# Performance work log

Hardware: AMD Instinct MI355X
Metric: run time of the kernel (lower is better)

The kernel has to match this reference:

```python
import jax, jax.numpy as jnp
import numpy as np

PI = 3.141592653589793


def _conv2d(x, w, b=None, pad=0, groups=1):
    out = jax.lax.conv_general_dilated(
        x, w, (1, 1), ((pad, pad), (pad, pad)),
        dimension_numbers=('NCHW', 'OIHW', 'NCHW'), feature_group_count=groups)
    if b is not None:
        out = out + b[None, :, None, None]
    return out


def _l2norm(x, eps=1e-12):
    # torch F.normalize(p=2, dim=1)
    n = jnp.sqrt(jnp.sum(x * x, axis=1, keepdims=True))
    return x / jnp.maximum(n, eps)


def dense_sift(x):
    # Kornia DenseSIFTDescriptor defaults: 8 angular bins, 4x4 spatial bins,
    # spatial_bin_size=4, stride=1, padding=1, rootsift=True, clipval=0.2.
    eps = 1e-10
    nbins = 8
    # SpatialGradient('diff', normalized=False) with replicate padding:
    px = jnp.pad(x, ((0, 0), (0, 0), (0, 0), (1, 1)), mode='edge')
    gx = px[..., 2:] - px[..., :-2]
    py = jnp.pad(x, ((0, 0), (0, 0), (1, 1), (0, 0)), mode='edge')
    gy = py[:, :, 2:, :] - py[:, :, :-2, :]
    mag = jnp.sqrt(gx * gx + gy * gy + eps)
    ori = jnp.arctan2(gy, gx + eps) + 2.0 * PI
    o_big = nbins * ori / (2.0 * PI)
    bo0f = jnp.floor(o_big)
    wo1 = o_big - bo0f
    bo0 = jnp.mod(bo0f, nbins)
    bo1 = jnp.mod(bo0 + 1.0, nbins)
    w0 = (1.0 - wo1) * mag
    w1 = wo1 * mag
    bins = jnp.arange(nbins, dtype=x.dtype).reshape(1, nbins, 1, 1)
    # soft-assign gradient magnitude into 8 orientation bins  (B,8,H,W)
    ang = (bo0 == bins) * w0 + (bo1 == bins) * w1
    # AvgPool2d(4, stride=1, pad=2, count_include_pad=True) -> (B,8,H+1,W+1)
    avg_k = jnp.ones((nbins, 1, 4, 4), x.dtype) / 16.0
    pooled = _conv2d(ang, avg_k, pad=2, groups=nbins)
    # PoolingConv: identity-reshape 4x4 kernel, pad=1 -> 16 shifted copies of 8 chans
    B, _, Hp, Wp = pooled.shape
    H, W = Hp - 1, Wp - 1
    pp = jnp.pad(pooled, ((0, 0), (0, 0), (1, 1), (1, 1)))
    shifts = jnp.stack(
        [pp[:, :, i:i + H, j:j + W] for i in range(4) for j in range(4)], axis=2)
    out = shifts.reshape(B, nbins * 16, H, W)  # channel n = d*16 + i*4 + j
    out = jnp.clip(_l2norm(out), 0.0, 0.2)
    out = _l2norm(out)
    # rootsift: sqrt(L1-normalize + eps)
    l1 = jnp.sum(jnp.abs(out), axis=1, keepdims=True)
    return jnp.sqrt(out / jnp.maximum(l1, 1e-12) + eps)


def joint_bilateral_blur(x, guidance, ksize=5, sigma_color=0.1, sigma_space=1.5):
    # Kornia joint_bilateral_blur, border='reflect', color_distance='l1'
    r = ksize // 2
    ax = jnp.arange(ksize, dtype=x.dtype) - r
    g1 = jnp.exp(-(ax * ax) / (2.0 * sigma_space ** 2))
    g1 = g1 / jnp.sum(g1)
    space_k = jnp.outer(g1, g1)
    H, W = x.shape[-2], x.shape[-1]
    px = jnp.pad(x, ((0, 0), (0, 0), (r, r), (r, r)), mode='reflect')
    pg = jnp.pad(guidance, ((0, 0), (0, 0), (r, r), (r, r)), mode='reflect')
    num = jnp.zeros_like(x)
    den = jnp.zeros((x.shape[0], 1, H, W), x.dtype)
    inv = -0.5 / (sigma_color ** 2)
    for dy in range(ksize):
        for dx in range(ksize):
            gw = pg[:, :, dy:dy + H, dx:dx + W]
            cd = jnp.square(jnp.sum(jnp.abs(gw - guidance), axis=1, keepdims=True))
            k = space_k[dy, dx] * jnp.exp(inv * cd)
            num = num + px[:, :, dy:dy + H, dx:dx + W] * k
            den = den + k
    return num / den


def setup_inputs() -> dict:
    key = jax.random.key(0)
    ks = jax.random.split(key, 7)
    B, H, W = 4, 270, 512
    x = jax.random.uniform(ks[0], (B, 1, H, W), dtype=jnp.float32)
    def winit(k, shape):
        fan_in = shape[1] * shape[2] * shape[3]
        return jax.random.normal(k, shape, dtype=jnp.float32) / np.sqrt(fan_in)
    return {
        'x': x,
        'conv1_w': winit(ks[1], (32, 128, 5, 5)),
        'conv1_b': jax.random.normal(ks[2], (32,), dtype=jnp.float32) * 0.01,
        'conv2_w': winit(ks[3], (8, 32, 3, 3)),
        'conv2_b': jax.random.normal(ks[4], (8,), dtype=jnp.float32) * 0.01,
        'conv3_w': winit(ks[5], (2, 8, 5, 5)),
        'conv3_b': jax.random.normal(ks[6], (2,), dtype=jnp.float32) * 0.01,
    }


def reference(x, conv1_w, conv1_b, conv2_w, conv2_b, conv3_w, conv3_b):
    orig = x
    f = dense_sift(x)
    f = jax.nn.relu(_conv2d(f, conv1_w, conv1_b, pad=2))
    f = jax.nn.relu(_conv2d(f, conv2_w, conv2_b, pad=1))
    f = _conv2d(f, conv3_w, conv3_b, pad=2)
    f = joint_bilateral_blur(f, jnp.concatenate([orig, orig], axis=1))
    u = f[:, 0]
    u = jnp.clip((u - u.min()) / (u.max() - u.min() + 1e-6), 0.0, 1.0)
    u = u * (0.436 * 2.0) - 0.436
    v = f[:, 1]
    v = jnp.clip((v - v.min()) / (v.max() - v.min() + 1e-6), 0.0, 1.0)
    v = v * (0.615 * 2.0) - 0.615
    y = orig[:, 0]
    r = y + 1.14 * v
    g = y - 0.396 * u - 0.581 * v
    b = y + 2.029 * u
    return jnp.stack([r, g, b], axis=1)
```

## Files before the change

kernel.cpp:

```cpp
#include <hip/hip_runtime.h>
#include <hip/hip_bf16.h>

typedef __hip_bfloat16 bf16;
typedef __attribute__((ext_vector_type(8))) short short8v;
typedef __attribute__((ext_vector_type(16))) float f32x16;

#define HH 270
#define WW 512
#define BB 4
#define HP 271
#define WP 513
#define NPIX (HH*WW)
#define NPOOL (HP*WP)
#define TWO_PI 6.28318530717958647692f
#define PLANE ((size_t)BB*NPIX*16)

__global__ void k_wprep(const float* __restrict__ w1, const float* __restrict__ w2,
                        const float* __restrict__ w3, short* __restrict__ apack,
                        float* __restrict__ wT2, float* __restrict__ wT3,
                        float* __restrict__ zp) {
    int stride = gridDim.x * blockDim.x;
    int t0 = blockIdx.x * blockDim.x + threadIdx.x;
    for (int i = t0; i < 1024; i += stride) zp[i] = 0.f;
    for (int i = t0; i < 8*25*64*8; i += stride) {
        int idx = i;
        int j    = idx & 7;  idx >>= 3;
        int lane = idx & 63; idx >>= 6;
        int t    = idx % 25;
        int ck   = idx / 25;
        int o = lane & 31;
        int c = ck*16 + (lane >> 5)*8 + j;
        float v = w1[o*3200 + c*25 + t];
        bf16 h = __float2bfloat16(v);
        apack[i] = *reinterpret_cast<short*>(&h);
    }
    for (int i = t0; i < 288*8;  i += stride) { int ck = i >> 3, o = i & 7;  wT2[i] = w2[o*288  + ck]; }
    for (int i = t0; i < 200*2;  i += stride) { int ck = i >> 1, o = i & 1;  wT3[i] = w3[o*200  + ck]; }
}

__global__ __launch_bounds__(256) void k_pool(const float* __restrict__ x,
                                              float* __restrict__ pooled) {
    __shared__ float hist[8][19][20];
    const int tx = threadIdx.x & 15, ty = threadIdx.x >> 4;
    const int j0 = blockIdx.x * 16, i0 = blockIdx.y * 16, b = blockIdx.z;
    const float* xb = x + (size_t)b * NPIX;

    for (int i = threadIdx.x; i < 8*19*20; i += 256) ((float*)hist)[i] = 0.f;
    __syncthreads();

    for (int i = threadIdx.x; i < 361; i += 256) {
        int lh = i / 19, lw = i - lh*19;
        int hh = i0 + lh - 2, ww = j0 + lw - 2;
        if (hh >= 0 && hh < HH && ww >= 0 && ww < WW) {
            float gx = xb[hh*WW + (ww+1 < WW ? ww+1 : WW-1)] - xb[hh*WW + (ww-1 >= 0 ? ww-1 : 0)];
            float gy = xb[(hh+1 < HH ? hh+1 : HH-1)*WW + ww] - xb[(hh-1 >= 0 ? hh-1 : 0)*WW + ww];
            float mag  = sqrtf(gx*gx + gy*gy + 1e-10f);
            float ori  = atan2f(gy, gx + 1e-10f) + TWO_PI;
            float obig = ori * (8.0f / TWO_PI);
            float b0f  = floorf(obig);
            float wo1  = obig - b0f;
            int ib0 = ((int)b0f) & 7;
            int ib1 = (ib0 + 1) & 7;
            hist[ib0][lh][lw] += (1.0f - wo1) * mag;
            hist[ib1][lh][lw] += wo1 * mag;
        }
    }
    __syncthreads();

    int i = i0 + ty, j = j0 + tx;
    if (i < HP && j < WP) {
        float a[8];
        #pragma unroll
        for (int c = 0; c < 8; ++c) a[c] = 0.f;
        #pragma unroll
        for (int di = 0; di < 4; ++di)
            #pragma unroll
            for (int dj = 0; dj < 4; ++dj) {
                #pragma unroll
                for (int c = 0; c < 8; ++c)
                    a[c] += hist[c][ty+di][tx+dj];
            }
        float* pb = pooled + (size_t)b*8*NPOOL + i*WP + j;
        const float s = 1.0f/16.0f;
        #pragma unroll
        for (int c = 0; c < 8; ++c) pb[c*NPOOL] = a[c]*s;
    }
}

__global__ __launch_bounds__(256) void k_feat(const float* __restrict__ pooled,
                                              short* __restrict__ f2) {
    __shared__ float T[8][19][19];
    const int tx = threadIdx.x & 15, ty = threadIdx.x >> 4;
    const int w0 = blockIdx.x * 16, h0 = blockIdx.y * 16, b = blockIdx.z;
    const float* pb = pooled + (size_t)b*8*NPOOL;

    for (int i = threadIdx.x; i < 8*361; i += 256) {
        int c = i / 361; int r = i - c*361; int lh = r / 19, lw = r - lh*19;
        int ph = h0 + lh - 1, pw = w0 + lw - 1;
        float v = 0.f;
        if (ph >= 0 && ph < HP && pw >= 0 && pw < WP)
            v = pb[c*NPOOL + ph*WP + pw];
        T[c][lh][lw] = v;
    }
    __syncthreads();

    float s2 = 0.f;
    #pragma unroll
    for (int c = 0; c < 8; ++c)
        #pragma unroll
        for (int i = 0; i < 4; ++i)
            #pragma unroll
            for (int j = 0; j < 4; ++j) {
                float u = T[c][ty+i][tx+j];
                s2 += u*u;
            }
    float inv1 = 1.0f / fmaxf(sqrtf(s2), 1e-12f);

    float sv2 = 0.f, sv1 = 0.f;
    #pragma unroll
    for (int c = 0; c < 8; ++c)
        #pragma unroll
        for (int i = 0; i < 4; ++i)
            #pragma unroll
            for (int j = 0; j < 4; ++j) {
                float u = T[c][ty+i][tx+j];
                float v = fminf(u*inv1, 0.2f);
                sv2 += v*v; sv1 += v;
            }
    float inv2  = 1.0f / fmaxf(sqrtf(sv2), 1e-12f);
    float invl1 = 1.0f / fmaxf(sv1 * inv2, 1e-12f);

    int outv[64];
    #pragma unroll
    for (int c = 0; c < 8; ++c)
        #pragma unroll
        for (int i = 0; i < 4; ++i)
            #pragma unroll
            for (int jj = 0; jj < 2; ++jj) {
                float u0 = T[c][ty+i][tx+jj*2];
                float u1 = T[c][ty+i][tx+jj*2+1];
                float v0 = fminf(u0*inv1, 0.2f) * inv2;
                float v1 = fminf(u1*inv1, 0.2f) * inv2;
                float fo0 = sqrtf(v0*invl1 + 1e-10f);
                float fo1 = sqrtf(v1*invl1 + 1e-10f);
                bf16 hb0 = __float2bfloat16(fo0);
                bf16 hb1 = __float2bfloat16(fo1);
                unsigned lo = *reinterpret_cast<unsigned short*>(&hb0);
                unsigned hi = *reinterpret_cast<unsigned short*>(&hb1);
                outv[c*8 + i*2 + jj] = (int)(lo | (hi << 16));
            }

    int h = h0 + ty, w = w0 + tx;
    if (h < HH) {
        const size_t pix = (size_t)b*NPIX + h*WW + w;
        #pragma unroll
        for (int ck = 0; ck < 8; ++ck) {
            int4* fb = reinterpret_cast<int4*>(f2 + (size_t)ck*PLANE + pix*16);
            int4 v0, v1;
            v0.x = outv[ck*8+0]; v0.y = outv[ck*8+1]; v0.z = outv[ck*8+2]; v0.w = outv[ck*8+3];
            v1.x = outv[ck*8+4]; v1.y = outv[ck*8+5]; v1.z = outv[ck*8+6]; v1.w = outv[ck*8+7];
            fb[0] = v0; fb[1] = v1;
        }
    }
}

__global__ __launch_bounds__(256) void k_conv1(const short* __restrict__ f2,
        const short* __restrict__ apack, const float* __restrict__ bias,
        short* __restrict__ c1o, const float* __restrict__ zp) {
    __shared__ short S[2][17408];
    const int tid = threadIdx.x;
    const int l   = tid & 63;
    const int wid = tid >> 6;
    const int n      = blockIdx.x;
    const int xcd    = n & 7;
    const int t_     = n >> 3;
    const int within = t_ & 7;
    const int g      = (t_ >> 3)*8 + xcd;
    const int b      = g / 34;
    const int ypair  = g - b*34;
    const int h0     = (ypair*2 + (within >> 2)) * 4;
    const int w0     = (within & 3) * 128;
    const int c32 = l & 31;
    const int ksel = l >> 5;

    f32x16 acc0 = {0.f};
    f32x16 acc1 = {0.f};
    f32x16 acc2 = {0.f};
    f32x16 acc3 = {0.f};

    auto STAGE = [&](int ck, int buf) {
        const short* plane = f2 + (size_t)ck*PLANE;
        for (int s = tid; s < 2176; s += 256) {
            int pr   = s / 272;
            int r    = s - pr*272;
            int px   = r >> 1;
            int half = r & 1;
            int gh = h0 + pr - 2, gw = w0 + px - 2;
            const void* src = (gh >= 0 && gh < HH && gw >= 0 && gw < WW)
                ? (const void*)(plane + (((size_t)b*HH + gh)*WW + gw)*16 + half*8)
                : (const void*)zp;
            short* dst = &S[buf][0] + (size_t)(s & ~63) * 8;
            __builtin_amdgcn_global_load_lds(
                (const __attribute__((address_space(1))) void*)src,
                (__attribute__((address_space(3))) void*)dst, 16, 0, 0);
        }
    };

    STAGE(0, 0);
    __syncthreads();

    for (int ck = 0; ck < 8; ++ck) {
        const int buf = ck & 1;
        if (ck < 7) STAGE(ck + 1, buf ^ 1);

        const short* Sb = &S[buf][0];
        #pragma unroll
        for (int kx = 0; kx < 5; ++kx) {
            const int px = wid*32 + c32 + kx;
            const short* bp = Sb + (size_t)px*16 + (size_t)ksel*8;
            short8v Bf[8];
            #pragma unroll
            for (int pr = 0; pr < 8; ++pr)
                Bf[pr] = *reinterpret_cast<const short8v*>(bp + pr*2176);
            #pragma unroll
            for (int ky = 0; ky < 5; ++ky) {
                const short* ap = apack + ((size_t)(ck*25 + ky*5 + kx)*64 + l)*8;
                short8v A = *reinterpret_cast<const short8v*>(ap);
                acc0 = __builtin_amdgcn_mfma_f32_32x32x16_bf16(A, Bf[ky+0], acc0, 0, 0, 0);
                acc1 = __builtin_amdgcn_mfma_f32_32x32x16_bf16(A, Bf[ky+1], acc1, 0, 0, 0);
                acc2 = __builtin_amdgcn_mfma_f32_32x32x16_bf16(A, Bf[ky+2], acc2, 0, 0, 0);
                acc3 = __builtin_amdgcn_mfma_f32_32x32x16_bf16(A, Bf[ky+3], acc3, 0, 0, 0);
            }
        }
        __syncthreads();
    }

    const int px = w0 + wid*32 + c32;
    #pragma unroll
    for (int r = 0; r < 4; ++r) {
        int h = h0 + r;
        if (h < HH) {
            const f32x16& A = (r==0) ? acc0 : (r==1) ? acc1 : (r==2) ? acc2 : acc3;
            const size_t rowbase = ((size_t)b*HH + h)*4;
            #pragma unroll
            for (int q = 0; q < 4; ++q) {
                short4 pk;
                short* pkp = (short*)&pk;
                #pragma unroll
                for (int j = 0; j < 4; ++j) {
                    float v = fmaxf(A[q*4 + j] + bias[q*8 + 4*ksel + j], 0.f);
                    bf16 hb = __float2bfloat16(v);
                    pkp[j] = *reinterpret_cast<short*>(&hb);
                }
                *reinterpret_cast<short4*>(c1o + ((rowbase + q)*WW + px)*8 + ksel*4) = pk;
            }
        }
    }
}

__global__ __launch_bounds__(256) void k_conv2(const short* __restrict__ in,
        const float* __restrict__ wT, const float* __restrict__ bias,
        float* __restrict__ out) {
    __shared__ float tile[8][18][18];
    int tx = threadIdx.x & 15, ty = threadIdx.x >> 4;
    int h0 = blockIdx.y * 16, w0 = blockIdx.x * 16, b = blockIdx.z;
    float acc[8];
    #pragma unroll
    for (int o = 0; o < 8; ++o) acc[o] = 0.f;

    for (int cc = 0; cc < 4; ++cc) {
        __syncthreads();
        for (int t = threadIdx.x; t < 324; t += 256) {
            int lh = t / 18, lw = t - lh*18;
            int gh = h0 + lh - 1, gw = w0 + lw - 1;
            if (gh >= 0 && gh < HH && gw >= 0 && gw < WW) {
                short8v v = *reinterpret_cast<const short8v*>(
                    in + (((size_t)b*HH + gh)*4 + cc)*WW*8 + (size_t)gw*8);
                #pragma unroll
                for (int c = 0; c < 8; ++c) {
                    unsigned u = ((unsigned)(unsigned short)v[c]) << 16;
                    tile[c][lh][lw] = *reinterpret_cast<float*>(&u);
                }
            } else {
                #pragma unroll
                for (int c = 0; c < 8; ++c) tile[c][lh][lw] = 0.f;
            }
        }
        __syncthreads();
        for (int c = 0; c < 8; ++c) {
            #pragma unroll
            for (int ky = 0; ky < 3; ++ky) {
                #pragma unroll
                for (int kx = 0; kx < 3; ++kx) {
                    float v = tile[c][ty+ky][tx+kx];
                    const float* wp = wT + (((cc*8+c)*9) + ky*3 + kx)*8;
                    #pragma unroll
                    for (int o = 0; o < 8; ++o) acc[o] = fmaf(v, wp[o], acc[o]);
                }
            }
        }
    }
    int h = h0 + ty, w = w0 + tx;
    if (h < HH) {
        float* op = out + (size_t)b*8*NPIX + h*WW + w;
        #pragma unroll
        for (int o = 0; o < 8; ++o) op[(size_t)o*NPIX] = fmaxf(acc[o] + bias[o], 0.f);
    }
}

__global__ __launch_bounds__(256) void k_conv3(const float* __restrict__ in,
        const float* __restrict__ wT, const float* __restrict__ bias,
        float* __restrict__ out) {
    __shared__ float tile[8][20][20];
    int tx = threadIdx.x & 15, ty = threadIdx.x >> 4;
    int h0 = blockIdx.y * 16, w0 = blockIdx.x * 16, b = blockIdx.z;
    float acc0 = 0.f, acc1 = 0.f;

    for (int t = threadIdx.x; t < 8*400; t += 256) {
        int c = t / 400; int r = t - c*400; int lh = r / 20, lw = r - lh*20;
        int gh = h0 + lh - 2, gw = w0 + lw - 2;
        float v = 0.f;
        if (gh >= 0 && gh < HH && gw >= 0 && gw < WW)
            v = in[((size_t)(b*8 + c))*NPIX + gh*WW + gw];
        tile[c][lh][lw] = v;
    }
    __syncthreads();
    for (int c = 0; c < 8; ++c) {
        for (int ky = 0; ky < 5; ++ky) {
            #pragma unroll
            for (int kx = 0; kx < 5; ++kx) {
                float v = tile[c][ty+ky][tx+kx];
                const float* wp = wT + ((c*25) + ky*5 + kx)*2;
                acc0 = fmaf(v, wp[0], acc0);
                acc1 = fmaf(v, wp[1], acc1);
            }
        }
    }
    int h = h0 + ty, w = w0 + tx;
    if (h < HH) {
        float* op = out + (size_t)b*2*NPIX + h*WW + w;
        op[0]    = acc0 + bias[0];
        op[NPIX] = acc1 + bias[1];
    }
}

__device__ __forceinline__ int refl(int i, int n) {
    if (i < 0) i = -i;
    if (i >= n) i = 2*n - 2 - i;
    return i;
}

__global__ void k_bilat(const float* __restrict__ c3, const float* __restrict__ x,
                        float* __restrict__ outb) {
    int idx = blockIdx.x * blockDim.x + threadIdx.x;
    if (idx >= BB*NPIX) return;
    int b = idx / NPIX;
    int p = idx - b*NPIX;
    int h = p / WW, w = p - h*WW;
    const float* xb = x + (size_t)b*NPIX;
    const float* f0 = c3 + (size_t)b*2*NPIX;
    const float* f1 = f0 + NPIX;

    float e1 = expf(-1.0f/4.5f), e2 = expf(-4.0f/4.5f);
    float sden = 1.0f + 2.f*e1 + 2.f*e2;
    float g1v[5] = { e2/sden, e1/sden, 1.0f/sden, e1/sden, e2/sden };

    float g = xb[p];
    float num0 = 0.f, num1 = 0.f, den = 0.f;
    #pragma unroll
    for (int dy = 0; dy < 5; ++dy) {
        int hh = refl(h + dy - 2, HH);
        #pragma unroll
        for (int dx = 0; dx < 5; ++dx) {
            int wc = refl(w + dx - 2, WW);
            float gs = xb[hh*WW + wc];
            float d = gs - g;
            float k = g1v[dy] * g1v[dx] * expf(-200.0f * d * d);
            num0 += f0[hh*WW + wc] * k;
            num1 += f1[hh*WW + wc] * k;
            den  += k;
        }
    }
    float invd = 1.0f / den;
    outb[(size_t)b*2*NPIX + p]        = num0 * invd;
    outb[(size_t)b*2*NPIX + NPIX + p] = num1 * invd;
}

__global__ void k_minmax1(const float* __restrict__ blur, float4* __restrict__ partial) {
    float umin = 3.0e38f, umax = -3.0e38f, vmin = 3.0e38f, vmax = -3.0e38f;
    for (int i = blockIdx.x*blockDim.x + threadIdx.x; i < BB*NPIX; i += gridDim.x*blockDim.x) {
        int b = i / NPIX; int p = i - b*NPIX;
        float u = blur[(size_t)b*2*NPIX + p];
        float v = blur[(size_t)b*2*NPIX + NPIX + p];
        umin = fminf(umin, u); umax = fmaxf(umax, u);
        vmin = fminf(vmin, v); vmax = fmaxf(vmax, v);
    }
    #pragma unroll
    for (int off = 32; off > 0; off >>= 1) {
        umin = fminf(umin, __shfl_down(umin, off));
        umax = fmaxf(umax, __shfl_down(umax, off));
        vmin = fminf(vmin, __shfl_down(vmin, off));
        vmax = fmaxf(vmax, __shfl_down(vmax, off));
    }
    __shared__ float4 sm[4];
    int lane = threadIdx.x & 63, wid = threadIdx.x >> 6;
    if (lane == 0) sm[wid] = make_float4(umin, umax, vmin, vmax);
    __syncthreads();
    if (threadIdx.x == 0) {
        float4 r = sm[0];
        for (int k = 1; k < 4; ++k) {
            r.x = fminf(r.x, sm[k].x); r.y = fmaxf(r.y, sm[k].y);
            r.z = fminf(r.z, sm[k].z); r.w = fmaxf(r.w, sm[k].w);
        }
        partial[blockIdx.x] = r;
    }
}

__global__ void k_minmax2(const float4* __restrict__ partial, float* __restrict__ sc) {
    float4 p = partial[threadIdx.x];
    #pragma unroll
    for (int off = 32; off > 0; off >>= 1) {
        p.x = fminf(p.x, __shfl_down(p.x, off));
        p.y = fmaxf(p.y, __shfl_down(p.y, off));
        p.z = fminf(p.z, __shfl_down(p.z, off));
        p.w = fmaxf(p.w, __shfl_down(p.w, off));
    }
    __shared__ float4 sm[2];
    if ((threadIdx.x & 63) == 0) sm[threadIdx.x >> 6] = p;
    __syncthreads();
    if (threadIdx.x == 0) {
        sc[0] = fminf(sm[0].x, sm[1].x);
        sc[1] = fmaxf(sm[0].y, sm[1].y);
        sc[2] = fminf(sm[0].z, sm[1].z);
        sc[3] = fmaxf(sm[0].w, sm[1].w);
    }
}

__global__ void k_final(const float* __restrict__ blur, const float* __restrict__ x,
                        const float* __restrict__ sc, float* __restrict__ out) {
    int idx = blockIdx.x * blockDim.x + threadIdx.x;
    if (idx >= BB*NPIX) return;
    int b = idx / NPIX;
    int p = idx - b*NPIX;
    float umin = sc[0], umax = sc[1], vmin = sc[2], vmax = sc[3];
    float u = blur[(size_t)b*2*NPIX + p];
    float v = blur[(size_t)b*2*NPIX + NPIX + p];
    u = fminf(fmaxf((u - umin) / (umax - umin + 1e-6f), 0.f), 1.f) * 0.872f - 0.436f;
    v = fminf(fmaxf((v - vmin) / (vmax - vmin + 1e-6f), 0.f), 1.f) * 1.23f  - 0.615f;
    float y = x[(size_t)b*NPIX + p];
    out[(size_t)(b*3+0)*NPIX + p] = y + 1.14f*v;
    out[(size_t)(b*3+1)*NPIX + p] = y - 0.396f*u - 0.581f*v;
    out[(size_t)(b*3+2)*NPIX + p] = y + 2.029f*u;
}

extern "C" void kernel_launch(void* const* d_in, const int* in_sizes, int n_in,
                              void* d_out, int out_size, void* d_ws, size_t ws_size,
                              hipStream_t stream) {
    const float* x  = (const float*)d_in[0];
    const float* w1 = (const float*)d_in[1];
    const float* b1 = (const float*)d_in[2];
    const float* w2 = (const float*)d_in[3];
    const float* b2 = (const float*)d_in[4];
    const float* w3 = (const float*)d_in[5];
    const float* b3 = (const float*)d_in[6];
    float* out = (float*)d_out;
    char* ws = (char*)d_ws;

    const size_t POOLED_OFF = 0;
    const size_t X_OFF      = 17795072;
    const size_t Y_OFF      = X_OFF + 141557760;
    const size_t AP_OFF     = Y_OFF + 35389440;
    const size_t WT2_OFF    = AP_OFF + 409600;
    const size_t WT3_OFF    = WT2_OFF + 9216;
    const size_t PART_OFF   = WT3_OFF + 3328;
    const size_t SC_OFF     = PART_OFF + 2048;
    const size_t ZP_OFF     = SC_OFF + 256;

    float*  pooled = (float*)(ws + POOLED_OFF);
    short*  f2     = (short*)(ws + X_OFF);
    float*  c2o    = (float*)(ws + X_OFF);
    float*  c3o    = (float*)(ws + X_OFF + 24000000);
    float*  blur   = (float*)(ws + X_OFF + 32000000);
    short*  c1o    = (short*)(ws + Y_OFF);
    short*  apack  = (short*)(ws + AP_OFF);
    float*  wT2    = (float*)(ws + WT2_OFF);
    float*  wT3    = (float*)(ws + WT3_OFF);
    float4* part   = (float4*)(ws + PART_OFF);
    float*  sc     = (float*)(ws + SC_OFF);
    float*  zp     = (float*)(ws + ZP_OFF);

    k_wprep<<<512, 256, 0, stream>>>(w1, w2, w3, apack, wT2, wT3, zp);

    dim3 pg((WP + 15)/16, (HP + 15)/16, BB);
    k_pool<<<pg, 256, 0, stream>>>(x, pooled);

    dim3 fg(WW/16, (HH + 15)/16, BB);
    k_feat<<<fg, 256, 0, stream>>>(pooled, f2);

    k_conv1<<<1088, 256, 0, stream>>>(f2, apack, b1, c1o, zp);

    dim3 cg(WW/16, (HH + 15)/16, BB);
    k_conv2<<<cg, 256, 0, stream>>>(c1o, wT2, b2, c2o);
    k_conv3<<<cg, 256, 0, stream>>>(c2o, wT3, b3, c3o);

    k_bilat<<<(BB*NPIX + 255)/256, 256, 0, stream>>>(c3o, x, blur);
    k_minmax1<<<128, 256, 0, stream>>>(blur, part);
    k_minmax2<<<1, 128, 0, stream>>>(part, sc);
    k_final<<<(BB*NPIX + 255)/256, 256, 0, stream>>>(blur, x, sc, out);
}
```

Baseline: 315.1 us.

## Load conv1 B fragments directly from global memory instead of LDS staging

Removes the double-buffered LDS staging of the input halo tile in the MFMA conv1 kernel. Each lane now reads its B fragments straight from global memory (relying on L1/L2 for the 5x5 halo reuse), with per-lane bounds predicates substituting a zero page for out-of-range taps. This drops the LDS footprint and the per-chunk barriers, which could raise occupancy. In exchange it gives up explicit reuse and async prefetch, adding redundant global loads and exposing load latency to the MFMA stream.

```diff
diff --git a/kernel.cpp b/kernel.cpp
--- a/kernel.cpp
+++ b/kernel.cpp
@@ -166,8 +166,7 @@
 
 __global__ __launch_bounds__(256) void k_conv1(const short* __restrict__ f2,
         const short* __restrict__ apack, const float* __restrict__ bias,
-        short* __restrict__ c1o, const float* __restrict__ zp) {
-    __shared__ short S[2][17408];
+        short* __restrict__ c1o, const short* __restrict__ zp16) {
     const int tid = threadIdx.x;
     const int l   = tid & 63;
     const int wid = tid >> 6;
@@ -183,45 +182,34 @@
     const int c32 = l & 31;
     const int ksel = l >> 5;
 
+    const int gw = w0 + wid*32 + c32 - 2;
+    bool vkx[5];
+    #pragma unroll
+    for (int kx = 0; kx < 5; ++kx) vkx[kx] = ((unsigned)(gw + kx) < WW);
+
     f32x16 acc0 = {0.f};
     f32x16 acc1 = {0.f};
     f32x16 acc2 = {0.f};
     f32x16 acc3 = {0.f};
 
-    auto STAGE = [&](int ck, int buf) {
+    for (int ck = 0; ck < 8; ++ck) {
         const short* plane = f2 + (size_t)ck*PLANE;
-        for (int s = tid; s < 2176; s += 256) {
-            int pr   = s / 272;
-            int r    = s - pr*272;
-            int px   = r >> 1;
-            int half = r & 1;
-            int gh = h0 + pr - 2, gw = w0 + px - 2;
-            const void* src = (gh >= 0 && gh < HH && gw >= 0 && gw < WW)
-                ? (const void*)(plane + (((size_t)b*HH + gh)*WW + gw)*16 + half*8)
-                : (const void*)zp;
-            short* dst = &S[buf][0] + (size_t)(s & ~63) * 8;
-            __builtin_amdgcn_global_load_lds(
-                (const __attribute__((address_space(1))) void*)src,
-                (__attribute__((address_space(3))) void*)dst, 16, 0, 0);
-        }
-    };
-
-    STAGE(0, 0);
-    __syncthreads();
-
-    for (int ck = 0; ck < 8; ++ck) {
-        const int buf = ck & 1;
-        if (ck < 7) STAGE(ck + 1, buf ^ 1);
-
-        const short* Sb = &S[buf][0];
+        const short* rp[8];
+        #pragma unroll
+        for (int pr = 0; pr < 8; ++pr) {
+            int gh = h0 + pr - 2;
+            rp[pr] = ((unsigned)gh < HH)
+                   ? plane + (((size_t)b*HH + gh)*WW + gw)*16 + ksel*8
+                   : zp16;
+        }
         #pragma unroll
         for (int kx = 0; kx < 5; ++kx) {
-            const int px = wid*32 + c32 + kx;
-            const short* bp = Sb + (size_t)px*16 + (size_t)ksel*8;
             short8v Bf[8];
             #pragma unroll
-            for (int pr = 0; pr < 8; ++pr)
-                Bf[pr] = *reinterpret_cast<const short8v*>(bp + pr*2176);
+            for (int pr = 0; pr < 8; ++pr) {
+                const short* p = vkx[kx] ? (rp[pr] + kx*16) : zp16;
+                Bf[pr] = *reinterpret_cast<const short8v*>(p);
+            }
             #pragma unroll
             for (int ky = 0; ky < 5; ++ky) {
                 const short* ap = apack + ((size_t)(ck*25 + ky*5 + kx)*64 + l)*8;
@@ -232,7 +220,6 @@
                 acc3 = __builtin_amdgcn_mfma_f32_32x32x16_bf16(A, Bf[ky+3], acc3, 0, 0, 0);
             }
         }
-        __syncthreads();
     }
 
     const int px = w0 + wid*32 + c32;
@@ -497,7 +484,7 @@
     dim3 fg(WW/16, (HH + 15)/16, BB);
     k_feat<<<fg, 256, 0, stream>>>(pooled, f2);
 
-    k_conv1<<<1088, 256, 0, stream>>>(f2, apack, b1, c1o, zp);
+    k_conv1<<<1088, 256, 0, stream>>>(f2, apack, b1, c1o, (const short*)zp);
 
     dim3 cg(WW/16, (HH + 15)/16, BB);
     k_conv2<<<cg, 256, 0, stream>>>(c1o, wT2, b2, c2o);
```

Result: slower. 336.2 us (+6.7%).
